# Kernel tuning notes

Measured on AMD Instinct MI355X. Metric: run time of the kernel, lower is better.

## Reference

```python
import jax, jax.numpy as jnp
import numpy as np

NF = 128
NH = 512


def setup_inputs() -> dict:
    key = jax.random.key(0)
    k_x, k_wx, k_wh = jax.random.split(key, 3)
    B, T = 4096, 64
    x = jax.random.normal(k_x, (B, T, NF), dtype=jnp.float32)
    # GlorotUniform init: limit = sqrt(6 / (fan_in + fan_out))
    lim_x = float(np.sqrt(6.0 / (NF + NH)))
    lim_h = float(np.sqrt(6.0 / (NH + NH)))
    wx = jax.random.uniform(k_wx, (NF, NH), minval=-lim_x, maxval=lim_x, dtype=jnp.float32)
    wh = jax.random.uniform(k_wh, (NH, NH), minval=-lim_h, maxval=lim_h, dtype=jnp.float32)
    b = jnp.zeros((1, NH), dtype=jnp.float32)
    return {"x": x, "wx": wx, "wh": wh, "b": b}


def reference(x, wx, wh, b):
    # x: [B, T, nf] -> final hidden state [B, nh]
    B = x.shape[0]
    # Precompute input projections for all timesteps in one big GEMM: [T, B, nh]
    xz = jnp.einsum('btf,fh->tbh', x, wx) + b

    def step(h, xz_t):
        h = jnp.tanh(xz_t + h @ wh)
        return h, None

    h0 = jnp.zeros((B, wh.shape[0]), dtype=x.dtype)
    h_final, _ = jax.lax.scan(step, h0, xz)
    return h_final
```

## Files before the change

### kernel.cpp

```cpp
#include <hip/hip_runtime.h>
#include <math.h>


#define T_STEPS 64
#define NFD     128
#define NHD     512
#define BR      16
#define THREADS 1024

typedef _Float16 half8 __attribute__((ext_vector_type(8)));
typedef _Float16 half2v __attribute__((ext_vector_type(2)));
typedef float float4v __attribute__((ext_vector_type(4)));

__global__ __launch_bounds__(256) void rnn_prep(
    const float* __restrict__ wh, const float* __restrict__ wx,
    _Float16* __restrict__ whp_hi, _Float16* __restrict__ whp_lo,
    _Float16* __restrict__ wxp_hi, _Float16* __restrict__ wxp_lo)
{
    int idx = blockIdx.x * 256 + threadIdx.x;
    {
        int j  = idx & 7;
        int l  = (idx >> 3) & 63;
        int nt = (idx >> 9) & 3;
        int kb = (idx >> 11) & 15;
        int w  = idx >> 15;
        int k  = kb * 32 + (l >> 4) * 8 + j;
        int n  = w * 64 + nt * 16 + (l & 15);
        float v = wh[k * NHD + n];
        _Float16 hi = (_Float16)v;
        whp_hi[idx] = hi;
        whp_lo[idx] = (_Float16)(v - (float)hi);
    }
    if (idx < 65536) {
        int j  = idx & 7;
        int l  = (idx >> 3) & 63;
        int nt = (idx >> 9) & 3;
        int kb = (idx >> 11) & 3;
        int w  = idx >> 13;
        int k  = kb * 32 + (l >> 4) * 8 + j;
        int n  = w * 64 + nt * 16 + (l & 15);
        float v = wx[k * NHD + n];
        _Float16 hi = (_Float16)v;
        wxp_hi[idx] = hi;
        wxp_lo[idx] = (_Float16)(v - (float)hi);
    }
}

__device__ __forceinline__ float fast_tanh(float v) {
    float xc = fminf(fmaxf(v, -9.0f), 9.0f);
    float e  = __builtin_amdgcn_exp2f(xc * 2.8853900817779268f);
    return (e - 1.0f) * __builtin_amdgcn_rcpf(e + 1.0f);
}

__global__ __launch_bounds__(THREADS, 4) void rnn_mfma(
    const float* __restrict__ x,
    const float* __restrict__ bias,
    const _Float16* __restrict__ whp_hi, const _Float16* __restrict__ whp_lo,
    const _Float16* __restrict__ wxp_hi, const _Float16* __restrict__ wxp_lo,
    float* __restrict__ out)
{
    __shared__ _Float16 s_fh[16 * 64 * 8];
    __shared__ _Float16 s_fl[16 * 64 * 8];
    __shared__ _Float16 s_xh[4 * 64 * 8];
    __shared__ _Float16 s_xl[4 * 64 * 8];
    __shared__ _Float16 s_w[16 * 7 * 64 * 8];

    const int tid  = (int)threadIdx.x;
    const int lane = tid & 63;
    const int w    = tid >> 6;
    const int m    = lane & 15;
    const int quad = lane >> 4;
    const int row0 = (int)blockIdx.x * BR;

    for (int i = tid; i < 16 * 64 * 8; i += THREADS) {
        s_fh[i] = (_Float16)0.f;
        s_fl[i] = (_Float16)0.f;
    }

    float bv[2];
    #pragma unroll
    for (int nt = 0; nt < 2; ++nt) bv[nt] = bias[w * 32 + nt * 16 + m];

    const half8* wxh = (const half8*)wxp_hi + (size_t)(w >> 1) * 1024 + (w & 1) * 128;
    const half8* wxl = (const half8*)wxp_lo + (size_t)(w >> 1) * 1024 + (w & 1) * 128;
    const half8* whh = (const half8*)whp_hi + (size_t)(w >> 1) * 4096 + (w & 1) * 128;
    const half8* whl = (const half8*)whp_lo + (size_t)(w >> 1) * 4096 + (w & 1) * 128;

    #pragma unroll
    for (int f = 0; f < 7; ++f) {
        int kb = f >> 1, nt = f & 1;
        half8 v = wxh[kb * 256 + nt * 64 + lane];
        *(half8*)&s_w[((w * 7 + f) * 64 + lane) * 8] = v;
    }

    const int xrow  = tid >> 6;
    const int xcol  = (tid & 63) * 2;
    const int xkb   = xcol >> 5;
    const int xkk   = xcol & 31;
    const int xoff  = (xkb * 64 + (xrow + 16 * (xkk >> 3))) * 8 + (xkk & 7);
    const float* xptr = x + (size_t)(row0 + xrow) * (T_STEPS * NFD) + xcol;
    float2 px = *(const float2*)xptr;

    const int eBase = w * 64 * 8 + (m & 7);
    const int eQ    = quad * 4;
    const int eHiM  = 16 * (m >> 3);

    for (int t = 0; t < T_STEPS; ++t) {
        half8 pbh31 = wxh[3 * 256 + 64 + lane];
        half8 pbl0[4], pbl1[4];
        #pragma unroll
        for (int kb = 0; kb < 4; ++kb) {
            pbl0[kb] = wxl[kb * 256 + lane];
            pbl1[kb] = wxl[kb * 256 + 64 + lane];
        }

        {
            half2v vh, vl;
            float xs[2] = {px.x, px.y};
            #pragma unroll
            for (int j = 0; j < 2; ++j) {
                _Float16 hi = (_Float16)xs[j];
                vh[j] = hi;
                vl[j] = (_Float16)(xs[j] - (float)hi);
            }
            *(half2v*)&s_xh[xoff] = vh;
            *(half2v*)&s_xl[xoff] = vl;
        }
        __syncthreads();

        if (t + 1 < T_STEPS) px = *(const float2*)(xptr + (t + 1) * NFD);

        float4v acc[2];
        #pragma unroll
        for (int nt = 0; nt < 2; ++nt) {
            acc[nt][0] = bv[nt]; acc[nt][1] = bv[nt];
            acc[nt][2] = bv[nt]; acc[nt][3] = bv[nt];
        }

        #pragma unroll
        for (int kb = 0; kb < 4; ++kb) {
            half8 ah = *(const half8*)&s_xh[(kb * 64 + lane) * 8];
            half8 al = *(const half8*)&s_xl[(kb * 64 + lane) * 8];
            half8 bh0 = *(const half8*)&s_w[((w * 7 + kb * 2) * 64 + lane) * 8];
            half8 bh1 = (kb < 3)
                ? *(const half8*)&s_w[((w * 7 + kb * 2 + 1) * 64 + lane) * 8]
                : pbh31;
            half8 bl0 = pbl0[kb];
            half8 bl1 = pbl1[kb];
            acc[0] = __builtin_amdgcn_mfma_f32_16x16x32_f16(ah, bh0, acc[0], 0, 0, 0);
            acc[0] = __builtin_amdgcn_mfma_f32_16x16x32_f16(al, bh0, acc[0], 0, 0, 0);
            acc[0] = __builtin_amdgcn_mfma_f32_16x16x32_f16(ah, bl0, acc[0], 0, 0, 0);
            acc[1] = __builtin_amdgcn_mfma_f32_16x16x32_f16(ah, bh1, acc[1], 0, 0, 0);
            acc[1] = __builtin_amdgcn_mfma_f32_16x16x32_f16(al, bh1, acc[1], 0, 0, 0);
            acc[1] = __builtin_amdgcn_mfma_f32_16x16x32_f16(ah, bl1, acc[1], 0, 0, 0);
        }

        #pragma unroll 4
        for (int kb = 0; kb < 16; ++kb) {
            half8 ah = *(const half8*)&s_fh[(kb * 64 + lane) * 8];
            half8 al = *(const half8*)&s_fl[(kb * 64 + lane) * 8];
            half8 bh0 = whh[kb * 256 + lane];
            half8 bh1 = whh[kb * 256 + 64 + lane];
            half8 bl0 = whl[kb * 256 + lane];
            half8 bl1 = whl[kb * 256 + 64 + lane];
            acc[0] = __builtin_amdgcn_mfma_f32_16x16x32_f16(ah, bh0, acc[0], 0, 0, 0);
            acc[0] = __builtin_amdgcn_mfma_f32_16x16x32_f16(al, bh0, acc[0], 0, 0, 0);
            acc[0] = __builtin_amdgcn_mfma_f32_16x16x32_f16(ah, bl0, acc[0], 0, 0, 0);
            acc[1] = __builtin_amdgcn_mfma_f32_16x16x32_f16(ah, bh1, acc[1], 0, 0, 0);
            acc[1] = __builtin_amdgcn_mfma_f32_16x16x32_f16(al, bh1, acc[1], 0, 0, 0);
            acc[1] = __builtin_amdgcn_mfma_f32_16x16x32_f16(ah, bl1, acc[1], 0, 0, 0);
        }

        __syncthreads();

        if (t == T_STEPS - 1) {
            #pragma unroll
            for (int nt = 0; nt < 2; ++nt)
                #pragma unroll
                for (int r = 0; r < 4; ++r)
                    out[(size_t)(row0 + quad * 4 + r) * NHD + w * 32 + nt * 16 + m] =
                        fast_tanh(acc[nt][r]);
        } else {
            #pragma unroll
            for (int nt = 0; nt < 2; ++nt) {
                #pragma unroll
                for (int r = 0; r < 4; ++r) {
                    float v = fast_tanh(acc[nt][r]);
                    _Float16 hi = (_Float16)v;
                    int fo = eBase + (eQ + r + 16 * (nt * 2) + eHiM) * 8;
                    s_fh[fo] = hi;
                    s_fl[fo] = (_Float16)(v - (float)hi);
                }
            }
        }
    }
}

extern "C" void kernel_launch(void* const* d_in, const int* in_sizes, int n_in,
                              void* d_out, int out_size, void* d_ws, size_t ws_size,
                              hipStream_t stream) {
    const float* x    = (const float*)d_in[0];
    const float* wx   = (const float*)d_in[1];
    const float* wh   = (const float*)d_in[2];
    const float* bias = (const float*)d_in[3];
    float* out = (float*)d_out;

    char* ws = (char*)d_ws;
    _Float16* whp_hi = (_Float16*)(ws);
    _Float16* whp_lo = (_Float16*)(ws + 524288);
    _Float16* wxp_hi = (_Float16*)(ws + 1048576);
    _Float16* wxp_lo = (_Float16*)(ws + 1048576 + 131072);

    rnn_prep<<<1024, 256, 0, stream>>>(wh, wx, whp_hi, whp_lo, wxp_hi, wxp_lo);

    const int B = in_sizes[0] / (T_STEPS * NFD);
    rnn_mfma<<<B / BR, THREADS, 0, stream>>>(x, bias, whp_hi, whp_lo, wxp_hi, wxp_lo, out);
}
```

Before: 795.1 us.

## Pin more weight fragments in registers and vectorize x staging loads

Loop-invariant Wx low/high fragments and the first two K-blocks of Wh are loaded once into registers before the time loop instead of being reloaded every step. The third Wh block is loaded early in each step to hide latency. The x tile is now staged by only 256 threads, each doing two float4 loads and one half8 LDS store, instead of every thread doing float2 loads with scattered half2 stores. This cuts per-step global and L2 weight traffic and LDS store count, but raises VGPR pressure under the 1024-thread, 4-block launch bound, which could cause spills.

```diff
diff --git a/kernel.cpp b/kernel.cpp
--- a/kernel.cpp
+++ b/kernel.cpp
@@ -9,7 +9,6 @@
 #define THREADS 1024
 
 typedef _Float16 half8 __attribute__((ext_vector_type(8)));
-typedef _Float16 half2v __attribute__((ext_vector_type(2)));
 typedef float float4v __attribute__((ext_vector_type(4)));
 
 __global__ __launch_bounds__(256) void rnn_prep(
@@ -52,6 +51,14 @@
     return (e - 1.0f) * __builtin_amdgcn_rcpf(e + 1.0f);
 }
 
+#define MFMA6(AH, AL, BH0, BH1, BL0, BL1)                                          \
+    acc[0] = __builtin_amdgcn_mfma_f32_16x16x32_f16((AH), (BH0), acc[0], 0, 0, 0); \
+    acc[0] = __builtin_amdgcn_mfma_f32_16x16x32_f16((AL), (BH0), acc[0], 0, 0, 0); \
+    acc[0] = __builtin_amdgcn_mfma_f32_16x16x32_f16((AH), (BL0), acc[0], 0, 0, 0); \
+    acc[1] = __builtin_amdgcn_mfma_f32_16x16x32_f16((AH), (BH1), acc[1], 0, 0, 0); \
+    acc[1] = __builtin_amdgcn_mfma_f32_16x16x32_f16((AL), (BH1), acc[1], 0, 0, 0); \
+    acc[1] = __builtin_amdgcn_mfma_f32_16x16x32_f16((AH), (BL1), acc[1], 0, 0, 0);
+
 __global__ __launch_bounds__(THREADS, 4) void rnn_mfma(
     const float* __restrict__ x,
     const float* __restrict__ bias,
@@ -93,42 +100,54 @@
         *(half8*)&s_w[((w * 7 + f) * 64 + lane) * 8] = v;
     }
 
-    const int xrow  = tid >> 6;
-    const int xcol  = (tid & 63) * 2;
-    const int xkb   = xcol >> 5;
-    const int xkk   = xcol & 31;
-    const int xoff  = (xkb * 64 + (xrow + 16 * (xkk >> 3))) * 8 + (xkk & 7);
-    const float* xptr = x + (size_t)(row0 + xrow) * (T_STEPS * NFD) + xcol;
-    float2 px = *(const float2*)xptr;
+    const half8 XH31 = wxh[3 * 256 + 64 + lane];
+    const half8 XL00 = wxl[0 * 256 + lane],      XL01 = wxl[0 * 256 + 64 + lane];
+    const half8 XL10 = wxl[1 * 256 + lane],      XL11 = wxl[1 * 256 + 64 + lane];
+    const half8 XL20 = wxl[2 * 256 + lane],      XL21 = wxl[2 * 256 + 64 + lane];
+    const half8 XL30 = wxl[3 * 256 + lane],      XL31 = wxl[3 * 256 + 64 + lane];
+    const half8 WH0h0 = whh[0 * 256 + lane],     WH0h1 = whh[0 * 256 + 64 + lane];
+    const half8 WH0l0 = whl[0 * 256 + lane],     WH0l1 = whl[0 * 256 + 64 + lane];
+    const half8 WH1h0 = whh[1 * 256 + lane],     WH1h1 = whh[1 * 256 + 64 + lane];
+    const half8 WH1l0 = whl[1 * 256 + lane],     WH1l1 = whl[1 * 256 + 64 + lane];
+
+    const int xi    = tid & 255;
+    const int xkb   = xi >> 6;
+    const int xlane = xi & 63;
+    const float* xptr = x + (size_t)(row0 + (xlane & 15)) * (T_STEPS * NFD)
+                          + xkb * 32 + (xlane >> 4) * 8;
+    float4v pxa, pxb;
+    if (tid < 256) {
+        pxa = *(const float4v*)xptr;
+        pxb = *(const float4v*)(xptr + 4);
+    }
 
     const int eBase = w * 64 * 8 + (m & 7);
     const int eQ    = quad * 4;
     const int eHiM  = 16 * (m >> 3);
 
     for (int t = 0; t < T_STEPS; ++t) {
-        half8 pbh31 = wxh[3 * 256 + 64 + lane];
-        half8 pbl0[4], pbl1[4];
-        #pragma unroll
-        for (int kb = 0; kb < 4; ++kb) {
-            pbl0[kb] = wxl[kb * 256 + lane];
-            pbl1[kb] = wxl[kb * 256 + 64 + lane];
-        }
-
-        {
-            half2v vh, vl;
-            float xs[2] = {px.x, px.y};
+        if (tid < 256) {
+            half8 vh, vl;
+            float xs[8] = {pxa[0], pxa[1], pxa[2], pxa[3],
+                           pxb[0], pxb[1], pxb[2], pxb[3]};
             #pragma unroll
-            for (int j = 0; j < 2; ++j) {
+            for (int j = 0; j < 8; ++j) {
                 _Float16 hi = (_Float16)xs[j];
                 vh[j] = hi;
                 vl[j] = (_Float16)(xs[j] - (float)hi);
             }
-            *(half2v*)&s_xh[xoff] = vh;
-            *(half2v*)&s_xl[xoff] = vl;
+            *(half8*)&s_xh[xi * 8] = vh;
+            *(half8*)&s_xl[xi * 8] = vl;
         }
         __syncthreads();
 
-        if (t + 1 < T_STEPS) px = *(const float2*)(xptr + (t + 1) * NFD);
+        if (t + 1 < T_STEPS && tid < 256) {
+            pxa = *(const float4v*)(xptr + (t + 1) * NFD);
+            pxb = *(const float4v*)(xptr + (t + 1) * NFD + 4);
+        }
+
+        half8 P2h0 = whh[2 * 256 + lane],      P2h1 = whh[2 * 256 + 64 + lane];
+        half8 P2l0 = whl[2 * 256 + lane],      P2l1 = whl[2 * 256 + 64 + lane];
 
         float4v acc[2];
         #pragma unroll
@@ -137,38 +156,51 @@
             acc[nt][2] = bv[nt]; acc[nt][3] = bv[nt];
         }
 
-        #pragma unroll
-        for (int kb = 0; kb < 4; ++kb) {
-            half8 ah = *(const half8*)&s_xh[(kb * 64 + lane) * 8];
-            half8 al = *(const half8*)&s_xl[(kb * 64 + lane) * 8];
-            half8 bh0 = *(const half8*)&s_w[((w * 7 + kb * 2) * 64 + lane) * 8];
-            half8 bh1 = (kb < 3)
-                ? *(const half8*)&s_w[((w * 7 + kb * 2 + 1) * 64 + lane) * 8]
-                : pbh31;
-            half8 bl0 = pbl0[kb];
-            half8 bl1 = pbl1[kb];
-            acc[0] = __builtin_amdgcn_mfma_f32_16x16x32_f16(ah, bh0, acc[0], 0, 0, 0);
-            acc[0] = __builtin_amdgcn_mfma_f32_16x16x32_f16(al, bh0, acc[0], 0, 0, 0);
-            acc[0] = __builtin_amdgcn_mfma_f32_16x16x32_f16(ah, bl0, acc[0], 0, 0, 0);
-            acc[1] = __builtin_amdgcn_mfma_f32_16x16x32_f16(ah, bh1, acc[1], 0, 0, 0);
-            acc[1] = __builtin_amdgcn_mfma_f32_16x16x32_f16(al, bh1, acc[1], 0, 0, 0);
-            acc[1] = __builtin_amdgcn_mfma_f32_16x16x32_f16(ah, bl1, acc[1], 0, 0, 0);
-        }
-
+        {
+            half8 ah, al;
+            ah = *(const half8*)&s_xh[(0 * 64 + lane) * 8];
+            al = *(const half8*)&s_xl[(0 * 64 + lane) * 8];
+            MFMA6(ah, al,
+                  *(const half8*)&s_w[((w * 7 + 0) * 64 + lane) * 8],
+                  *(const half8*)&s_w[((w * 7 + 1) * 64 + lane) * 8], XL00, XL01);
+            ah = *(const half8*)&s_xh[(1 * 64 + lane) * 8];
+            al = *(const half8*)&s_xl[(1 * 64 + lane) * 8];
+            MFMA6(ah, al,
+                  *(const half8*)&s_w[((w * 7 + 2) * 64 + lane) * 8],
+                  *(const half8*)&s_w[((w * 7 + 3) * 64 + lane) * 8], XL10, XL11);
+            ah = *(const half8*)&s_xh[(2 * 64 + lane) * 8];
+            al = *(const half8*)&s_xl[(2 * 64 + lane) * 8];
+            MFMA6(ah, al,
+                  *(const half8*)&s_w[((w * 7 + 4) * 64 + lane) * 8],
+                  *(const half8*)&s_w[((w * 7 + 5) * 64 + lane) * 8], XL20, XL21);
+            ah = *(const half8*)&s_xh[(3 * 64 + lane) * 8];
+            al = *(const half8*)&s_xl[(3 * 64 + lane) * 8];
+            MFMA6(ah, al,
+                  *(const half8*)&s_w[((w * 7 + 6) * 64 + lane) * 8],
+                  XH31, XL30, XL31);
+        }
+
+        {
+            half8 ah, al;
+            ah = *(const half8*)&s_fh[(0 * 64 + lane) * 8];
+            al = *(const half8*)&s_fl[(0 * 64 + lane) * 8];
+            MFMA6(ah, al, WH0h0, WH0h1, WH0l0, WH0l1);
+            ah = *(const half8*)&s_fh[(1 * 64 + lane) * 8];
+            al = *(const half8*)&s_fl[(1 * 64 + lane) * 8];
+            MFMA6(ah, al, WH1h0, WH1h1, WH1l0, WH1l1);
+            ah = *(const half8*)&s_fh[(2 * 64 + lane) * 8];
+            al = *(const half8*)&s_fl[(2 * 64 + lane) * 8];
+            MFMA6(ah, al, P2h0, P2h1, P2l0, P2l1);
+        }
         #pragma unroll 4
-        for (int kb = 0; kb < 16; ++kb) {
-            half8 ah = *(const half8*)&s_fh[(kb * 64 + lane) * 8];
-            half8 al = *(const half8*)&s_fl[(kb * 64 + lane) * 8];
+        for (int kb = 3; kb < 16; ++kb) {
+            half8 ah  = *(const half8*)&s_fh[(kb * 64 + lane) * 8];
+            half8 al  = *(const half8*)&s_fl[(kb * 64 + lane) * 8];
             half8 bh0 = whh[kb * 256 + lane];
             half8 bh1 = whh[kb * 256 + 64 + lane];
             half8 bl0 = whl[kb * 256 + lane];
             half8 bl1 = whl[kb * 256 + 64 + lane];
-            acc[0] = __builtin_amdgcn_mfma_f32_16x16x32_f16(ah, bh0, acc[0], 0, 0, 0);
-            acc[0] = __builtin_amdgcn_mfma_f32_16x16x32_f16(al, bh0, acc[0], 0, 0, 0);
-            acc[0] = __builtin_amdgcn_mfma_f32_16x16x32_f16(ah, bl0, acc[0], 0, 0, 0);
-            acc[1] = __builtin_amdgcn_mfma_f32_16x16x32_f16(ah, bh1, acc[1], 0, 0, 0);
-            acc[1] = __builtin_amdgcn_mfma_f32_16x16x32_f16(al, bh1, acc[1], 0, 0, 0);
-            acc[1] = __builtin_amdgcn_mfma_f32_16x16x32_f16(ah, bl1, acc[1], 0, 0, 0);
+            MFMA6(ah, al, bh0, bh1, bl0, bl1);
         }
 
         __syncthreads();
```

Measured after the change: 2.479 ms. +211.7%, slower.
